# Kernel tuning notes

Hardware: AMD Instinct MI355X
Metric: run time of the kernel (lower is better)

## Reference

```python
import jax, jax.numpy as jnp
import numpy as np

NUM_HEADS = 8
HEAD_DIM = 64
EMBED = NUM_HEADS * HEAD_DIM  # 512


def setup_inputs() -> dict:
    key = jax.random.key(0)
    ks = jax.random.split(key, 8)
    B, S = 4, 2048
    s = 1.0 / np.sqrt(HEAD_DIM)
    so = 1.0 / np.sqrt(EMBED)
    return {
        "queries": jax.random.normal(ks[0], (B, S, EMBED), jnp.float32),
        "keys": jax.random.normal(ks[1], (B, S, EMBED), jnp.float32),
        "values": jax.random.normal(ks[2], (B, S, EMBED), jnp.float32),
        "Wq": jax.random.uniform(ks[3], (HEAD_DIM, HEAD_DIM), jnp.float32, -s, s),
        "Wk": jax.random.uniform(ks[4], (HEAD_DIM, HEAD_DIM), jnp.float32, -s, s),
        "Wv": jax.random.uniform(ks[5], (HEAD_DIM, HEAD_DIM), jnp.float32, -s, s),
        "Wo": jax.random.uniform(ks[6], (EMBED, EMBED), jnp.float32, -so, so),
        "bo": jax.random.uniform(ks[7], (EMBED,), jnp.float32, -so, so),
    }


def reference(queries, keys, values, Wq, Wk, Wv, Wo, bo):
    B, Sq, _ = queries.shape
    # Faithful to source: keys/values are (buggily) reshaped from `queries`;
    # with equal seq lens this means k/v come from the queries tensor.
    q = queries.reshape(B, Sq, NUM_HEADS, HEAD_DIM)
    k = q
    v = q
    # per-head linear: torch Linear(x) = x @ W.T
    q = jnp.einsum('bshd,ed->bshe', q, Wq)
    k = jnp.einsum('bshd,ed->bshe', k, Wk)
    v = jnp.einsum('bshd,ed->bshe', v, Wv)
    sim = jnp.einsum('bqhd,bkhd->bhqk', q, k)  # [B,H,Sq,Sk]
    attn = jax.nn.softmax(sim * (1.0 / np.sqrt(HEAD_DIM)), axis=-1)
    out = jnp.einsum('bhqk,bkhd->bqhd', attn, v)
    out = out.reshape(B, Sq, EMBED)
    return out @ Wo.T + bo
```

## Files before the change

### kernel.cpp

```cpp
#include <hip/hip_runtime.h>
#include <cstddef>

#define S_ 2048
#define E_ 512

typedef __attribute__((ext_vector_type(8)))  short bf16x8;
typedef __attribute__((ext_vector_type(16))) float f32x16;

__device__ __forceinline__ unsigned short f2bf(float f) {
    union { float f; unsigned u; } v; v.f = f;
    return (unsigned short)((v.u + 0x7FFFu + ((v.u >> 16) & 1u)) >> 16);
}
__device__ __forceinline__ unsigned pk2bf(float a, float b) {
    union { float f; unsigned u; } x, y; x.f = a; y.f = b;
    return __builtin_amdgcn_perm(y.u + 0x8000u, x.u + 0x8000u, 0x07060302u);
}

__global__ __launch_bounds__(256) void prep_w(const float* __restrict__ Wq,
                                              const float* __restrict__ Wk,
                                              const float* __restrict__ Wo,
                                              const float* __restrict__ Wv,
                                              unsigned short* __restrict__ GT,
                                              unsigned short* __restrict__ W2) {
    int bi = blockIdx.x;
    if (bi < 16) {
        int idx = bi * 256 + threadIdx.x;
        int c = idx >> 6, d = idx & 63;
        float acc = 0.f;
#pragma unroll 8
        for (int e = 0; e < 64; ++e) acc += Wq[e * 64 + d] * Wk[e * 64 + c];
        GT[c * 64 + d] = f2bf(acc * 0.18033688011112042f);
    } else {
        int idx = (bi - 16) * 256 + threadIdx.x;
        int e = idx >> 9, f = idx & 511;
        int h = f >> 6, c = f & 63;
        const float* wo = Wo + e * 512 + h * 64;
        float acc = 0.f;
#pragma unroll 8
        for (int d = 0; d < 64; ++d) acc += wo[d] * Wv[d * 64 + c];
        W2[idx] = f2bf(acc);
    }
}

__global__ __launch_bounds__(256) void prep_X(const float* __restrict__ X,
                                              unsigned short* __restrict__ Xbf,
                                              unsigned short* __restrict__ XTg) {
    __shared__ unsigned short T[64][72];
    const int tid = threadIdx.x;
    const int st = blockIdx.x & 31, h = (blockIdx.x >> 5) & 7, b = blockIdx.x >> 8;
    const int s0 = st * 64;
    const int j = tid >> 2, g = tid & 3;
    const float* src = X + ((size_t)(b * S_ + s0 + j) * E_) + h * 64 + g * 16;
    unsigned short us[16];
#pragma unroll
    for (int i = 0; i < 16; i += 4) {
        float4 f = *(const float4*)(src + i);
        us[i] = f2bf(f.x); us[i + 1] = f2bf(f.y);
        us[i + 2] = f2bf(f.z); us[i + 3] = f2bf(f.w);
    }
    size_t xb = ((size_t)(b * S_ + s0 + j) * E_) + h * 64 + g * 16;
    *(uint4*)&Xbf[xb]     = *(uint4*)&us[0];
    *(uint4*)&Xbf[xb + 8] = *(uint4*)&us[8];
#pragma unroll
    for (int i = 0; i < 16; ++i) T[g * 16 + i][j] = us[i];
    __syncthreads();
    const int d = tid >> 2;
    const int pm[16] = {0,1,2,3,8,9,10,11,4,5,6,7,12,13,14,15};
    unsigned short o[16];
#pragma unroll
    for (int i = 0; i < 16; ++i) o[i] = T[d][g * 16 + pm[i]];
    size_t tb = ((size_t)((b * 8 + h) * 64 + d)) * S_ + s0 + g * 16;
    *(uint4*)&XTg[tb]     = *(uint4*)&o[0];
    *(uint4*)&XTg[tb + 8] = *(uint4*)&o[8];
}

__global__ __launch_bounds__(256, 4) void attn_mfma(const unsigned short* __restrict__ Xbf,
                                                    const unsigned short* __restrict__ XTg,
                                                    const unsigned short* __restrict__ GT,
                                                    unsigned short* __restrict__ AObf) {
    __shared__ union SM {
        unsigned short Q[128][72];
        struct { unsigned short Xrm[64][72], XT[64][72]; } c;
        unsigned short AOt[128][72];
    } sm;

    const int tid = threadIdx.x;
    const int w = tid >> 6, lane = tid & 63;
    const int lm = lane & 31, lh = lane >> 5;
    const int qt = blockIdx.x & 15, h = (blockIdx.x >> 4) & 7, b = blockIdx.x >> 7;
    const int s0 = qt * 128;

    {
        const int r = tid >> 1, c = (tid & 1) * 32;
        const unsigned short* src = Xbf + ((size_t)(b * S_ + s0 + r)) * E_ + h * 64 + c;
#pragma unroll
        for (int u = 0; u < 4; ++u) *(uint4*)&sm.Q[r][c + u * 8] = *(const uint4*)(src + u * 8);
    }
    __syncthreads();

    bf16x8 Ufrag[4];
    {
        f32x16 ua[2];
#pragma unroll
        for (int nt = 0; nt < 2; ++nt)
#pragma unroll
            for (int i = 0; i < 16; ++i) ua[nt][i] = 0.f;
#pragma unroll
        for (int ks = 0; ks < 4; ++ks) {
            bf16x8 aQ = *(const bf16x8*)&sm.Q[32 * w + lm][ks * 16 + lh * 8];
#pragma unroll
            for (int nt = 0; nt < 2; ++nt) {
                bf16x8 bG = *(const bf16x8*)&GT[(lm + 32 * nt) * 64 + ks * 16 + lh * 8];
                ua[nt] = __builtin_amdgcn_mfma_f32_32x32x16_bf16(aQ, bG, ua[nt], 0, 0, 0);
            }
        }
#pragma unroll
        for (int nt = 0; nt < 2; ++nt)
#pragma unroll
            for (int r = 0; r < 16; ++r)
                sm.Q[32 * w + (r & 3) + 8 * (r >> 2) + 4 * lh][lm + 32 * nt] = f2bf(ua[nt][r]);
#pragma unroll
        for (int ks = 0; ks < 4; ++ks)
            Ufrag[ks] = *(const bf16x8*)&sm.Q[32 * w + lm][ks * 16 + lh * 8];
    }

    float lsum = 0.f;
    f32x16 AO[2];
#pragma unroll
    for (int mt = 0; mt < 2; ++mt)
#pragma unroll
        for (int i = 0; i < 16; ++i) AO[mt][i] = 0.f;

    const unsigned short* srcX = Xbf + ((size_t)(b * S_ + (tid >> 2))) * E_ + h * 64 + (tid & 3) * 16;
    const unsigned short* srcT = XTg + ((size_t)((b * 8 + h) * 64 + (tid >> 2))) * S_ + (tid & 3) * 16;

    for (int sk = 0; sk < S_; sk += 64) {
        __syncthreads();
        {
            const unsigned short* sx = srcX + (size_t)sk * E_;
            const int r = tid >> 2, c = (tid & 3) * 16;
            *(uint4*)&sm.c.Xrm[r][c]     = *(const uint4*)sx;
            *(uint4*)&sm.c.Xrm[r][c + 8] = *(const uint4*)(sx + 8);
            const unsigned short* st = srcT + sk;
            *(uint4*)&sm.c.XT[r][c]      = *(const uint4*)st;
            *(uint4*)&sm.c.XT[r][c + 8]  = *(const uint4*)(st + 8);
        }
        __syncthreads();

        f32x16 sc[2];
#pragma unroll
        for (int mt = 0; mt < 2; ++mt)
#pragma unroll
            for (int i = 0; i < 16; ++i) sc[mt][i] = 0.f;
#pragma unroll
        for (int ks = 0; ks < 4; ++ks)
#pragma unroll
            for (int mt = 0; mt < 2; ++mt) {
                bf16x8 aX = *(const bf16x8*)&sm.c.Xrm[32 * mt + lm][ks * 16 + lh * 8];
                sc[mt] = __builtin_amdgcn_mfma_f32_32x32x16_bf16(aX, Ufrag[ks], sc[mt], 0, 0, 0);
            }

        unsigned up[16];
#pragma unroll
        for (int mt = 0; mt < 2; ++mt)
#pragma unroll
            for (int qq = 0; qq < 4; ++qq) {
                float p0 = exp2f(sc[mt][qq * 4 + 0]);
                float p1 = exp2f(sc[mt][qq * 4 + 1]);
                float p2 = exp2f(sc[mt][qq * 4 + 2]);
                float p3 = exp2f(sc[mt][qq * 4 + 3]);
                lsum += (p0 + p1) + (p2 + p3);
                up[mt * 8 + 2 * qq]     = pk2bf(p0, p1);
                up[mt * 8 + 2 * qq + 1] = pk2bf(p2, p3);
            }

#pragma unroll
        for (int js = 0; js < 4; ++js) {
            union { unsigned u[4]; bf16x8 v; } bP;
            bP.u[0] = up[js * 4 + 0]; bP.u[1] = up[js * 4 + 1];
            bP.u[2] = up[js * 4 + 2]; bP.u[3] = up[js * 4 + 3];
#pragma unroll
            for (int mt = 0; mt < 2; ++mt) {
                bf16x8 aT = *(const bf16x8*)&sm.c.XT[32 * mt + lm][js * 16 + lh * 8];
                AO[mt] = __builtin_amdgcn_mfma_f32_32x32x16_bf16(aT, bP.v, AO[mt], 0, 0, 0);
            }
        }
    }

    lsum += __shfl_xor(lsum, 32);
    float linv = 1.0f / lsum;
    __syncthreads();
#pragma unroll
    for (int mt = 0; mt < 2; ++mt)
#pragma unroll
        for (int qq = 0; qq < 4; ++qq) {
            int d0 = 32 * mt + 8 * qq + 4 * lh;
            *(unsigned*)&sm.AOt[32 * w + lm][d0] =
                pk2bf(AO[mt][qq * 4 + 0] * linv, AO[mt][qq * 4 + 1] * linv);
            *(unsigned*)&sm.AOt[32 * w + lm][d0 + 2] =
                pk2bf(AO[mt][qq * 4 + 2] * linv, AO[mt][qq * 4 + 3] * linv);
        }
    __syncthreads();
    {
        const int r = tid >> 1, c = (tid & 1) * 32;
        unsigned short* dst = AObf + ((size_t)(b * S_ + s0 + r)) * E_ + h * 64 + c;
#pragma unroll
        for (int u = 0; u < 4; ++u)
            *(uint4*)(dst + u * 8) = *(const uint4*)&sm.AOt[r][c + u * 8];
    }
}

__global__ __launch_bounds__(256) void out_gemm_bf(const unsigned short* __restrict__ A,
                                                   const unsigned short* __restrict__ W2,
                                                   const float* __restrict__ bo,
                                                   float* __restrict__ out) {
    __shared__ unsigned short At[64][72];
    __shared__ unsigned short Bt[128][72];
    const int tid = threadIdx.x;
    const int w = tid >> 6, lane = tid & 63;
    const int lm = lane & 31, lh = lane >> 5;
    const int et = blockIdx.x & 3, rt = blockIdx.x >> 2;
    const int r0 = rt * 64, e0 = et * 128;
    f32x16 acc[2];
#pragma unroll
    for (int mt = 0; mt < 2; ++mt)
#pragma unroll
        for (int i = 0; i < 16; ++i) acc[mt][i] = 0.f;

    for (int k0 = 0; k0 < 512; k0 += 64) {
        __syncthreads();
        {
            const int r = tid >> 2, c = (tid & 3) * 16;
            const unsigned short* sa = A + (size_t)(r0 + r) * 512 + k0 + c;
            *(uint4*)&At[r][c]     = *(const uint4*)sa;
            *(uint4*)&At[r][c + 8] = *(const uint4*)(sa + 8);
            const int r2 = tid >> 1, c2 = (tid & 1) * 32;
            const unsigned short* sb = W2 + (size_t)(e0 + r2) * 512 + k0 + c2;
#pragma unroll
            for (int u = 0; u < 4; ++u)
                *(uint4*)&Bt[r2][c2 + u * 8] = *(const uint4*)(sb + u * 8);
        }
        __syncthreads();
#pragma unroll
        for (int ks = 0; ks < 4; ++ks) {
            bf16x8 bW = *(const bf16x8*)&Bt[32 * w + lm][ks * 16 + lh * 8];
#pragma unroll
            for (int mt = 0; mt < 2; ++mt) {
                bf16x8 aA = *(const bf16x8*)&At[32 * mt + lm][ks * 16 + lh * 8];
                acc[mt] = __builtin_amdgcn_mfma_f32_32x32x16_bf16(aA, bW, acc[mt], 0, 0, 0);
            }
        }
    }
    float bv = bo[e0 + 32 * w + lm];
#pragma unroll
    for (int mt = 0; mt < 2; ++mt)
#pragma unroll
        for (int r = 0; r < 16; ++r) {
            int srow = r0 + 32 * mt + (r & 3) + 8 * (r >> 2) + 4 * lh;
            out[(size_t)srow * 512 + e0 + 32 * w + lm] = acc[mt][r] + bv;
        }
}

extern "C" void kernel_launch(void* const* d_in, const int* in_sizes, int n_in,
                              void* d_out, int out_size, void* d_ws, size_t ws_size,
                              hipStream_t stream) {
    (void)in_sizes; (void)n_in; (void)out_size; (void)ws_size;
    const float* X  = (const float*)d_in[0];
    const float* Wq = (const float*)d_in[3];
    const float* Wk = (const float*)d_in[4];
    const float* Wv = (const float*)d_in[5];
    const float* Wo = (const float*)d_in[6];
    const float* bo = (const float*)d_in[7];

    float* ws = (float*)d_ws;
    unsigned short* W2bf = (unsigned short*)ws;
    unsigned short* GT   = (unsigned short*)(ws + 131072);
    unsigned short* Xbf  = (unsigned short*)(ws + 133120);
    unsigned short* XTg  = (unsigned short*)(ws + 133120 + 2097152);
    unsigned short* AObf = (unsigned short*)(ws + 133120 + 4194304);

    prep_w     <<<1040, 256, 0, stream>>>(Wq, Wk, Wo, Wv, GT, W2bf);
    prep_X     <<<1024, 256, 0, stream>>>(X, Xbf, XTg);
    attn_mfma  <<<512,  256, 0, stream>>>(Xbf, XTg, GT, AObf);
    out_gemm_bf<<<512,  256, 0, stream>>>(AObf, W2bf, bo, (float*)d_out);
}
```

Baseline: 181.1 us.

## Split attention over key halves, double-buffer LDS, merge prep kernels

The attention kernel now splits the key range into two halves, doubling the grid to 1024 blocks. Each half writes unnormalized bf16 partial outputs and row sums, and the output GEMM combines the two partials and normalizes them while loading its A tile. The key loop double-buffers LDS with register prefetch so it needs one barrier per tile instead of two. The two prep kernels are fused into one launch, and the output GEMM moves to 64x64 tiles with 1024 blocks. The split adds partial-output traffic and an extra bf16 rounding before the merge. Skipping the max subtraction, as the code already did, is safe only while the partial sums stay in range.

```diff
diff --git a/kernel.cpp b/kernel.cpp
--- a/kernel.cpp
+++ b/kernel.cpp
@@ -3,6 +3,7 @@
 
 #define S_ 2048
 #define E_ 512
+#define SPLIT_STRIDE 4194304u
 
 typedef __attribute__((ext_vector_type(8)))  short bf16x8;
 typedef __attribute__((ext_vector_type(16))) float f32x16;
@@ -15,23 +16,59 @@
     union { float f; unsigned u; } x, y; x.f = a; y.f = b;
     return __builtin_amdgcn_perm(y.u + 0x8000u, x.u + 0x8000u, 0x07060302u);
 }
-
-__global__ __launch_bounds__(256) void prep_w(const float* __restrict__ Wq,
-                                              const float* __restrict__ Wk,
-                                              const float* __restrict__ Wo,
-                                              const float* __restrict__ Wv,
-                                              unsigned short* __restrict__ GT,
-                                              unsigned short* __restrict__ W2) {
-    int bi = blockIdx.x;
-    if (bi < 16) {
-        int idx = bi * 256 + threadIdx.x;
+__device__ __forceinline__ float bflo(unsigned u) {
+    union { unsigned u; float f; } v; v.u = u << 16; return v.f;
+}
+__device__ __forceinline__ float bfhi(unsigned u) {
+    union { unsigned u; float f; } v; v.u = u & 0xffff0000u; return v.f;
+}
+
+__global__ __launch_bounds__(256) void prep_all(const float* __restrict__ X,
+                                                const float* __restrict__ Wq,
+                                                const float* __restrict__ Wk,
+                                                const float* __restrict__ Wo,
+                                                const float* __restrict__ Wv,
+                                                unsigned short* __restrict__ Xbf,
+                                                unsigned short* __restrict__ XTg,
+                                                unsigned short* __restrict__ GT,
+                                                unsigned short* __restrict__ W2) {
+    __shared__ unsigned short T[64][72];
+    const int bi = blockIdx.x, tid = threadIdx.x;
+    if (bi < 1024) {
+        const int st = bi & 31, h = (bi >> 5) & 7, b = bi >> 8;
+        const int s0 = st * 64;
+        const int j = tid >> 2, g = tid & 3;
+        const float* src = X + ((size_t)(b * S_ + s0 + j) * E_) + h * 64 + g * 16;
+        unsigned short us[16];
+#pragma unroll
+        for (int i = 0; i < 16; i += 4) {
+            float4 f = *(const float4*)(src + i);
+            us[i] = f2bf(f.x); us[i + 1] = f2bf(f.y);
+            us[i + 2] = f2bf(f.z); us[i + 3] = f2bf(f.w);
+        }
+        size_t xb = ((size_t)(b * S_ + s0 + j) * E_) + h * 64 + g * 16;
+        *(uint4*)&Xbf[xb]     = *(uint4*)&us[0];
+        *(uint4*)&Xbf[xb + 8] = *(uint4*)&us[8];
+#pragma unroll
+        for (int i = 0; i < 16; ++i) T[g * 16 + i][j] = us[i];
+        __syncthreads();
+        const int d = tid >> 2;
+        const int pm[16] = {0,1,2,3,8,9,10,11,4,5,6,7,12,13,14,15};
+        unsigned short o[16];
+#pragma unroll
+        for (int i = 0; i < 16; ++i) o[i] = T[d][g * 16 + pm[i]];
+        size_t tb = ((size_t)((b * 8 + h) * 64 + d)) * S_ + s0 + g * 16;
+        *(uint4*)&XTg[tb]     = *(uint4*)&o[0];
+        *(uint4*)&XTg[tb + 8] = *(uint4*)&o[8];
+    } else if (bi < 1040) {
+        int idx = (bi - 1024) * 256 + tid;
         int c = idx >> 6, d = idx & 63;
         float acc = 0.f;
 #pragma unroll 8
         for (int e = 0; e < 64; ++e) acc += Wq[e * 64 + d] * Wk[e * 64 + c];
         GT[c * 64 + d] = f2bf(acc * 0.18033688011112042f);
     } else {
-        int idx = (bi - 16) * 256 + threadIdx.x;
+        int idx = (bi - 1040) * 256 + tid;
         int e = idx >> 9, f = idx & 511;
         int h = f >> 6, c = f & 63;
         const float* wo = Wo + e * 512 + h * 64;
@@ -42,53 +79,23 @@
     }
 }
 
-__global__ __launch_bounds__(256) void prep_X(const float* __restrict__ X,
-                                              unsigned short* __restrict__ Xbf,
-                                              unsigned short* __restrict__ XTg) {
-    __shared__ unsigned short T[64][72];
-    const int tid = threadIdx.x;
-    const int st = blockIdx.x & 31, h = (blockIdx.x >> 5) & 7, b = blockIdx.x >> 8;
-    const int s0 = st * 64;
-    const int j = tid >> 2, g = tid & 3;
-    const float* src = X + ((size_t)(b * S_ + s0 + j) * E_) + h * 64 + g * 16;
-    unsigned short us[16];
-#pragma unroll
-    for (int i = 0; i < 16; i += 4) {
-        float4 f = *(const float4*)(src + i);
-        us[i] = f2bf(f.x); us[i + 1] = f2bf(f.y);
-        us[i + 2] = f2bf(f.z); us[i + 3] = f2bf(f.w);
-    }
-    size_t xb = ((size_t)(b * S_ + s0 + j) * E_) + h * 64 + g * 16;
-    *(uint4*)&Xbf[xb]     = *(uint4*)&us[0];
-    *(uint4*)&Xbf[xb + 8] = *(uint4*)&us[8];
-#pragma unroll
-    for (int i = 0; i < 16; ++i) T[g * 16 + i][j] = us[i];
-    __syncthreads();
-    const int d = tid >> 2;
-    const int pm[16] = {0,1,2,3,8,9,10,11,4,5,6,7,12,13,14,15};
-    unsigned short o[16];
-#pragma unroll
-    for (int i = 0; i < 16; ++i) o[i] = T[d][g * 16 + pm[i]];
-    size_t tb = ((size_t)((b * 8 + h) * 64 + d)) * S_ + s0 + g * 16;
-    *(uint4*)&XTg[tb]     = *(uint4*)&o[0];
-    *(uint4*)&XTg[tb + 8] = *(uint4*)&o[8];
-}
-
 __global__ __launch_bounds__(256, 4) void attn_mfma(const unsigned short* __restrict__ Xbf,
                                                     const unsigned short* __restrict__ XTg,
                                                     const unsigned short* __restrict__ GT,
-                                                    unsigned short* __restrict__ AObf) {
+                                                    unsigned short* __restrict__ AOp,
+                                                    float* __restrict__ Lp) {
     __shared__ union SM {
         unsigned short Q[128][72];
-        struct { unsigned short Xrm[64][72], XT[64][72]; } c;
+        unsigned short cbuf[2][2 * 64 * 72];
         unsigned short AOt[128][72];
     } sm;
 
     const int tid = threadIdx.x;
     const int w = tid >> 6, lane = tid & 63;
     const int lm = lane & 31, lh = lane >> 5;
-    const int qt = blockIdx.x & 15, h = (blockIdx.x >> 4) & 7, b = blockIdx.x >> 7;
-    const int s0 = qt * 128;
+    const int qt = blockIdx.x & 15, h = (blockIdx.x >> 4) & 7, b = (blockIdx.x >> 7) & 3;
+    const int split = blockIdx.x >> 9;
+    const int s0 = qt * 128, sk0 = split * (S_ / 2);
 
     {
         const int r = tid >> 1, c = (tid & 1) * 32;
@@ -123,6 +130,25 @@
         for (int ks = 0; ks < 4; ++ks)
             Ufrag[ks] = *(const bf16x8*)&sm.Q[32 * w + lm][ks * 16 + lh * 8];
     }
+    __syncthreads();
+
+    const int rr = tid >> 2, cc = (tid & 3) * 16;
+    const unsigned short* srcX = Xbf + ((size_t)(b * S_ + rr)) * E_ + h * 64 + cc;
+    const unsigned short* srcT = XTg + ((size_t)((b * 8 + h) * 64 + rr)) * S_ + cc;
+    const int ldsOff = rr * 72 + cc;
+
+    unsigned short* bufR = sm.cbuf[0];
+    unsigned short* bufW = sm.cbuf[1];
+
+    {
+        const unsigned short* sx = srcX + (size_t)sk0 * E_;
+        const unsigned short* st = srcT + sk0;
+        *(uint4*)(bufR + ldsOff)           = *(const uint4*)sx;
+        *(uint4*)(bufR + ldsOff + 8)       = *(const uint4*)(sx + 8);
+        *(uint4*)(bufR + 64 * 72 + ldsOff)     = *(const uint4*)st;
+        *(uint4*)(bufR + 64 * 72 + ldsOff + 8) = *(const uint4*)(st + 8);
+    }
+    __syncthreads();
 
     float lsum = 0.f;
     f32x16 AO[2];
@@ -131,21 +157,15 @@
 #pragma unroll
         for (int i = 0; i < 16; ++i) AO[mt][i] = 0.f;
 
-    const unsigned short* srcX = Xbf + ((size_t)(b * S_ + (tid >> 2))) * E_ + h * 64 + (tid & 3) * 16;
-    const unsigned short* srcT = XTg + ((size_t)((b * 8 + h) * 64 + (tid >> 2))) * S_ + (tid & 3) * 16;
-
-    for (int sk = 0; sk < S_; sk += 64) {
-        __syncthreads();
-        {
-            const unsigned short* sx = srcX + (size_t)sk * E_;
-            const int r = tid >> 2, c = (tid & 3) * 16;
-            *(uint4*)&sm.c.Xrm[r][c]     = *(const uint4*)sx;
-            *(uint4*)&sm.c.Xrm[r][c + 8] = *(const uint4*)(sx + 8);
-            const unsigned short* st = srcT + sk;
-            *(uint4*)&sm.c.XT[r][c]      = *(const uint4*)st;
-            *(uint4*)&sm.c.XT[r][c + 8]  = *(const uint4*)(st + 8);
-        }
-        __syncthreads();
+    for (int ck = 0; ck < 16; ++ck) {
+        uint4 pre0, pre1, pre2, pre3;
+        const bool have = (ck < 15);
+        if (have) {
+            const unsigned short* sx = srcX + (size_t)(sk0 + (ck + 1) * 64) * E_;
+            const unsigned short* st = srcT + sk0 + (ck + 1) * 64;
+            pre0 = *(const uint4*)sx;  pre1 = *(const uint4*)(sx + 8);
+            pre2 = *(const uint4*)st;  pre3 = *(const uint4*)(st + 8);
+        }
 
         f32x16 sc[2];
 #pragma unroll
@@ -156,7 +176,7 @@
         for (int ks = 0; ks < 4; ++ks)
 #pragma unroll
             for (int mt = 0; mt < 2; ++mt) {
-                bf16x8 aX = *(const bf16x8*)&sm.c.Xrm[32 * mt + lm][ks * 16 + lh * 8];
+                bf16x8 aX = *(const bf16x8*)(bufR + (32 * mt + lm) * 72 + ks * 16 + lh * 8);
                 sc[mt] = __builtin_amdgcn_mfma_f32_32x32x16_bf16(aX, Ufrag[ks], sc[mt], 0, 0, 0);
             }
 
@@ -181,84 +201,103 @@
             bP.u[2] = up[js * 4 + 2]; bP.u[3] = up[js * 4 + 3];
 #pragma unroll
             for (int mt = 0; mt < 2; ++mt) {
-                bf16x8 aT = *(const bf16x8*)&sm.c.XT[32 * mt + lm][js * 16 + lh * 8];
+                bf16x8 aT = *(const bf16x8*)(bufR + 64 * 72 + (32 * mt + lm) * 72 + js * 16 + lh * 8);
                 AO[mt] = __builtin_amdgcn_mfma_f32_32x32x16_bf16(aT, bP.v, AO[mt], 0, 0, 0);
             }
         }
+
+        if (have) {
+            *(uint4*)(bufW + ldsOff)               = pre0;
+            *(uint4*)(bufW + ldsOff + 8)           = pre1;
+            *(uint4*)(bufW + 64 * 72 + ldsOff)     = pre2;
+            *(uint4*)(bufW + 64 * 72 + ldsOff + 8) = pre3;
+        }
+        __syncthreads();
+        unsigned short* t = bufR; bufR = bufW; bufW = t;
     }
 
     lsum += __shfl_xor(lsum, 32);
-    float linv = 1.0f / lsum;
-    __syncthreads();
 #pragma unroll
     for (int mt = 0; mt < 2; ++mt)
 #pragma unroll
         for (int qq = 0; qq < 4; ++qq) {
             int d0 = 32 * mt + 8 * qq + 4 * lh;
             *(unsigned*)&sm.AOt[32 * w + lm][d0] =
-                pk2bf(AO[mt][qq * 4 + 0] * linv, AO[mt][qq * 4 + 1] * linv);
+                pk2bf(AO[mt][qq * 4 + 0], AO[mt][qq * 4 + 1]);
             *(unsigned*)&sm.AOt[32 * w + lm][d0 + 2] =
-                pk2bf(AO[mt][qq * 4 + 2] * linv, AO[mt][qq * 4 + 3] * linv);
+                pk2bf(AO[mt][qq * 4 + 2], AO[mt][qq * 4 + 3]);
         }
     __syncthreads();
     {
         const int r = tid >> 1, c = (tid & 1) * 32;
-        unsigned short* dst = AObf + ((size_t)(b * S_ + s0 + r)) * E_ + h * 64 + c;
+        unsigned short* dst = AOp + (size_t)split * SPLIT_STRIDE
+                            + ((size_t)(b * S_ + s0 + r)) * E_ + h * 64 + c;
 #pragma unroll
         for (int u = 0; u < 4; ++u)
             *(uint4*)(dst + u * 8) = *(const uint4*)&sm.AOt[r][c + u * 8];
     }
-}
-
-__global__ __launch_bounds__(256) void out_gemm_bf(const unsigned short* __restrict__ A,
+    if (lane < 32)
+        Lp[((size_t)(split * 4 + b) * 8 + h) * S_ + s0 + 32 * w + lm] = lsum;
+}
+
+__global__ __launch_bounds__(256) void out_gemm_bf(const unsigned short* __restrict__ AOp,
+                                                   const float* __restrict__ Lp,
                                                    const unsigned short* __restrict__ W2,
                                                    const float* __restrict__ bo,
                                                    float* __restrict__ out) {
     __shared__ unsigned short At[64][72];
-    __shared__ unsigned short Bt[128][72];
+    __shared__ unsigned short Bt[64][72];
     const int tid = threadIdx.x;
     const int w = tid >> 6, lane = tid & 63;
     const int lm = lane & 31, lh = lane >> 5;
-    const int et = blockIdx.x & 3, rt = blockIdx.x >> 2;
-    const int r0 = rt * 64, e0 = et * 128;
-    f32x16 acc[2];
-#pragma unroll
-    for (int mt = 0; mt < 2; ++mt)
-#pragma unroll
-        for (int i = 0; i < 16; ++i) acc[mt][i] = 0.f;
+    const int et = blockIdx.x & 7, rt = blockIdx.x >> 3;
+    const int r0 = rt * 64, e0 = et * 64;
+    const int rr = tid >> 2, cc = (tid & 3) * 16;
+    const int srow = r0 + rr, bb = srow >> 11, ss = srow & 2047;
+
+    f32x16 acc;
+#pragma unroll
+    for (int i = 0; i < 16; ++i) acc[i] = 0.f;
 
     for (int k0 = 0; k0 < 512; k0 += 64) {
+        const int hh = k0 >> 6;
+        const float linv = 1.0f / (Lp[((size_t)(bb)*8 + hh) * S_ + ss] +
+                                   Lp[((size_t)(4 + bb) * 8 + hh) * S_ + ss]);
         __syncthreads();
         {
-            const int r = tid >> 2, c = (tid & 3) * 16;
-            const unsigned short* sa = A + (size_t)(r0 + r) * 512 + k0 + c;
-            *(uint4*)&At[r][c]     = *(const uint4*)sa;
-            *(uint4*)&At[r][c + 8] = *(const uint4*)(sa + 8);
-            const int r2 = tid >> 1, c2 = (tid & 1) * 32;
-            const unsigned short* sb = W2 + (size_t)(e0 + r2) * 512 + k0 + c2;
-#pragma unroll
-            for (int u = 0; u < 4; ++u)
-                *(uint4*)&Bt[r2][c2 + u * 8] = *(const uint4*)(sb + u * 8);
+            const unsigned short* a0 = AOp + (size_t)srow * 512 + k0 + cc;
+            const unsigned short* a1 = a0 + SPLIT_STRIDE;
+            uint4 u0 = *(const uint4*)a0, u0b = *(const uint4*)(a0 + 8);
+            uint4 u1 = *(const uint4*)a1, u1b = *(const uint4*)(a1 + 8);
+            uint4 o, ob;
+            o.x  = pk2bf((bflo(u0.x) + bflo(u1.x)) * linv, (bfhi(u0.x) + bfhi(u1.x)) * linv);
+            o.y  = pk2bf((bflo(u0.y) + bflo(u1.y)) * linv, (bfhi(u0.y) + bfhi(u1.y)) * linv);
+            o.z  = pk2bf((bflo(u0.z) + bflo(u1.z)) * linv, (bfhi(u0.z) + bfhi(u1.z)) * linv);
+            o.w  = pk2bf((bflo(u0.w) + bflo(u1.w)) * linv, (bfhi(u0.w) + bfhi(u1.w)) * linv);
+            ob.x = pk2bf((bflo(u0b.x) + bflo(u1b.x)) * linv, (bfhi(u0b.x) + bfhi(u1b.x)) * linv);
+            ob.y = pk2bf((bflo(u0b.y) + bflo(u1b.y)) * linv, (bfhi(u0b.y) + bfhi(u1b.y)) * linv);
+            ob.z = pk2bf((bflo(u0b.z) + bflo(u1b.z)) * linv, (bfhi(u0b.z) + bfhi(u1b.z)) * linv);
+            ob.w = pk2bf((bflo(u0b.w) + bflo(u1b.w)) * linv, (bfhi(u0b.w) + bfhi(u1b.w)) * linv);
+            *(uint4*)&At[rr][cc]     = o;
+            *(uint4*)&At[rr][cc + 8] = ob;
+            const unsigned short* sb = W2 + (size_t)(e0 + rr) * 512 + k0 + cc;
+            *(uint4*)&Bt[rr][cc]     = *(const uint4*)sb;
+            *(uint4*)&Bt[rr][cc + 8] = *(const uint4*)(sb + 8);
         }
         __syncthreads();
 #pragma unroll
         for (int ks = 0; ks < 4; ++ks) {
-            bf16x8 bW = *(const bf16x8*)&Bt[32 * w + lm][ks * 16 + lh * 8];
-#pragma unroll
-            for (int mt = 0; mt < 2; ++mt) {
-                bf16x8 aA = *(const bf16x8*)&At[32 * mt + lm][ks * 16 + lh * 8];
-                acc[mt] = __builtin_amdgcn_mfma_f32_32x32x16_bf16(aA, bW, acc[mt], 0, 0, 0);
-            }
-        }
-    }
-    float bv = bo[e0 + 32 * w + lm];
-#pragma unroll
-    for (int mt = 0; mt < 2; ++mt)
-#pragma unroll
-        for (int r = 0; r < 16; ++r) {
-            int srow = r0 + 32 * mt + (r & 3) + 8 * (r >> 2) + 4 * lh;
-            out[(size_t)srow * 512 + e0 + 32 * w + lm] = acc[mt][r] + bv;
-        }
+            bf16x8 aA = *(const bf16x8*)&At[32 * (w & 1) + lm][ks * 16 + lh * 8];
+            bf16x8 bW = *(const bf16x8*)&Bt[32 * (w >> 1) + lm][ks * 16 + lh * 8];
+            acc = __builtin_amdgcn_mfma_f32_32x32x16_bf16(aA, bW, acc, 0, 0, 0);
+        }
+    }
+    const float bv = bo[e0 + 32 * (w >> 1) + lm];
+#pragma unroll
+    for (int r = 0; r < 16; ++r) {
+        int orow = r0 + 32 * (w & 1) + (r & 3) + 8 * (r >> 2) + 4 * lh;
+        out[(size_t)orow * 512 + e0 + 32 * (w >> 1) + lm] = acc[r] + bv;
+    }
 }
 
 extern "C" void kernel_launch(void* const* d_in, const int* in_sizes, int n_in,
@@ -276,11 +315,11 @@
     unsigned short* W2bf = (unsigned short*)ws;
     unsigned short* GT   = (unsigned short*)(ws + 131072);
     unsigned short* Xbf  = (unsigned short*)(ws + 133120);
-    unsigned short* XTg  = (unsigned short*)(ws + 133120 + 2097152);
-    unsigned short* AObf = (unsigned short*)(ws + 133120 + 4194304);
-
-    prep_w     <<<1040, 256, 0, stream>>>(Wq, Wk, Wo, Wv, GT, W2bf);
-    prep_X     <<<1024, 256, 0, stream>>>(X, Xbf, XTg);
-    attn_mfma  <<<512,  256, 0, stream>>>(Xbf, XTg, GT, AObf);
-    out_gemm_bf<<<512,  256, 0, stream>>>(AObf, W2bf, bo, (float*)d_out);
-}
+    unsigned short* XTg  = (unsigned short*)(ws + 2230272);
+    unsigned short* AOp  = (unsigned short*)(ws + 4327424);
+    float*          Lp   = ws + 8521728;
+
+    prep_all   <<<2064, 256, 0, stream>>>(X, Wq, Wk, Wo, Wv, Xbf, XTg, GT, W2bf);
+    attn_mfma  <<<1024, 256, 0, stream>>>(Xbf, XTg, GT, AOp, Lp);
+    out_gemm_bf<<<1024, 256, 0, stream>>>(AOp, Lp, W2bf, bo, (float*)d_out);
+}
```

New measurement: 182.2 us. About the same (+0.6%).
